# Kernel tuning notes

Hardware: AMD Instinct MI355X
Metric: run time of the kernel (lower is better)

## Reference

```python
import jax, jax.numpy as jnp
import numpy as np
from functools import partial

B, T, H, W = 8, 256, 64, 64
D_MODEL, N_LAYERS, D_STATE = 256, 6, 16
D_INNER = 2 * D_MODEL
DT_RANK = 16  # ceil(256/16)
D_CONV = 4
CNN_Z = 32


def setup_inputs() -> dict:
    key = jax.random.key(0)
    ks = iter(jax.random.split(key, 64))
    r = lambda shape, s=0.02: jax.random.normal(next(ks), shape, dtype=jnp.float32) * s
    inp = {
        'x': jax.random.normal(next(ks), (B, T, 1, H, W), dtype=jnp.float32),
        # frozen CNN spatial encoder (1->16->32->32, stride-2 convs, global avg pool)
        'cnn_w1': r((16, 1, 3, 3)), 'cnn_b1': jnp.zeros((16,)),
        'cnn_w2': r((32, 16, 3, 3)), 'cnn_b2': jnp.zeros((32,)),
        'cnn_w3': r((32, 32, 3, 3)), 'cnn_b3': jnp.zeros((32,)),
        # fc_s2t: 32 -> 256
        'fc_w': r((D_MODEL, CNN_Z)), 'fc_b': jnp.zeros((D_MODEL,)),
        # Mamba, stacked over layers
        'norm_w': jnp.ones((N_LAYERS, D_MODEL)),
        'in_proj_w': r((N_LAYERS, 2 * D_INNER, D_MODEL)),
        'conv1d_w': r((N_LAYERS, D_INNER, D_CONV)),
        'conv1d_b': jnp.zeros((N_LAYERS, D_INNER)),
        'x_proj_w': r((N_LAYERS, DT_RANK + 2 * D_STATE, D_INNER)),
        'dt_proj_w': r((N_LAYERS, D_INNER, DT_RANK)),
        'dt_proj_b': jnp.full((N_LAYERS, D_INNER), -4.6),  # softplus ~ 0.01
        'A_log': jnp.tile(jnp.log(jnp.arange(1, D_STATE + 1, dtype=jnp.float32))[None, None, :], (N_LAYERS, D_INNER, 1)),
        'Dp': jnp.ones((N_LAYERS, D_INNER)),
        'out_proj_w': r((N_LAYERS, D_MODEL, D_INNER)),
        'norm_f_w': jnp.ones((D_MODEL,)),
        # prediction head: 256 -> 64 -> 1
        'head_w1': r((D_MODEL // 4, D_MODEL)), 'head_b1': jnp.zeros((D_MODEL // 4,)),
        'head_w2': r((1, D_MODEL // 4)), 'head_b2': jnp.zeros((1,)),
    }
    return inp


def _conv2d(x, w, b, stride):
    y = jax.lax.conv_general_dilated(x, w, (stride, stride), 'SAME',
                                     dimension_numbers=('NCHW', 'OIHW', 'NCHW'))
    return jax.nn.relu(y + b[None, :, None, None])


def _rmsnorm(x, w, eps=1e-5):
    return x * jax.lax.rsqrt(jnp.mean(x * x, axis=-1, keepdims=True) + eps) * w


def _selective_scan(u, delta, A, Bm, Cm, Dvec):
    # u,delta: (B,L,E); A: (E,N); Bm,Cm: (B,L,N); D: (E,)
    deltaA = jnp.exp(delta[..., None] * A)                       # (B,L,E,N)
    deltaBu = delta[..., None] * Bm[:, :, None, :] * u[..., None]  # (B,L,E,N)

    def step(h, inputs):
        dA, dBu, c = inputs
        h = dA * h + dBu                    # (B,E,N)
        y = jnp.einsum('ben,bn->be', h, c)  # (B,E)
        return h, y

    h0 = jnp.zeros((u.shape[0], u.shape[2], A.shape[1]), u.dtype)
    xs = (deltaA.transpose(1, 0, 2, 3), deltaBu.transpose(1, 0, 2, 3), Cm.transpose(1, 0, 2))
    _, ys = jax.lax.scan(step, h0, xs)
    return ys.transpose(1, 0, 2) + u * Dvec  # (B,L,E)


def _mamba_block(x, nw, ipw, cw, cb, xpw, dpw, dpb, a_log, dvec, opw):
    b, l, d = x.shape
    xz = _rmsnorm(x, nw) @ ipw.T                 # (B,L,2E)
    xin, z = jnp.split(xz, 2, axis=-1)
    # causal depthwise conv1d, kernel 4
    xc = xin.transpose(0, 2, 1)                  # (B,E,L)
    xc = jax.lax.conv_general_dilated(xc, cw[:, None, :], (1,), [(D_CONV - 1, 0)],
                                      feature_group_count=D_INNER,
                                      dimension_numbers=('NCH', 'OIH', 'NCH'))
    xin = jax.nn.silu((xc + cb[None, :, None]).transpose(0, 2, 1))  # (B,L,E)
    dbc = xin @ xpw.T                             # (B,L,dtr+2N)
    dt, Bm, Cm = jnp.split(dbc, [DT_RANK, DT_RANK + D_STATE], axis=-1)
    delta = jax.nn.softplus(dt @ dpw.T + dpb)     # (B,L,E)
    A = -jnp.exp(a_log)                           # (E,N)
    y = _selective_scan(xin, delta, A, Bm, Cm, dvec)
    y = y * jax.nn.silu(z)
    return x + y @ opw.T


def reference(x, cnn_w1, cnn_b1, cnn_w2, cnn_b2, cnn_w3, cnn_b3, fc_w, fc_b,
              norm_w, in_proj_w, conv1d_w, conv1d_b, x_proj_w, dt_proj_w, dt_proj_b,
              A_log, Dp, out_proj_w, norm_f_w, head_w1, head_b1, head_w2, head_b2):
    b, t = x.shape[:2]
    # spatial encoder per frame
    f = x.reshape(b * t, 1, H, W)
    f = _conv2d(f, cnn_w1, cnn_b1, 2)
    f = _conv2d(f, cnn_w2, cnn_b2, 2)
    f = _conv2d(f, cnn_w3, cnn_b3, 2)
    z1 = jnp.mean(f, axis=(2, 3)).reshape(b, t, CNN_Z)   # (B,T,32)
    h = z1 @ fc_w.T + fc_b                                # (B,T,256)
    for i in range(N_LAYERS):
        h = _mamba_block(h, norm_w[i], in_proj_w[i], conv1d_w[i], conv1d_b[i],
                         x_proj_w[i], dt_proj_w[i], dt_proj_b[i], A_log[i], Dp[i], out_proj_w[i])
    z2 = _rmsnorm(h, norm_f_w)
    hh = jax.nn.gelu(z2 @ head_w1.T + head_b1)
    logits = hh @ head_w2.T + head_b2                     # (B,T,1)
    w = jax.nn.softmax(logits, axis=-2)
    w = w.at[:, 0, 0].set(0.0)
    return w
```

## Files before the change

kernel.cpp:

```cpp
#include <hip/hip_runtime.h>
#include <hip/hip_bf16.h>
#include <math.h>

#define Bb 8
#define Tt 256
#define DM 256
#define DI 512
#define NL 6
#define DS 16
#define DTR 16

#define OFF_H     0u
#define OFF_XZ    524288u
#define OFF_U     2621440u
#define OFF_DBC   3670016u
#define OFF_DELTA 3768320u
#define OFF_HH    4816896u
#define OFF_LOGIT 4947968u
#define OFF_XNB   4950016u
#define OFF_UB    5212160u
#define OFF_YBF   5736448u
#define OFF_WIP   6260736u
#define OFF_WXP   7047168u
#define OFF_WOP   7120896u

__device__ __forceinline__ float siluf(float x) { return x / (1.f + __expf(-x)); }

typedef __attribute__((ext_vector_type(8))) short bf16x8;
typedef __attribute__((ext_vector_type(4))) short bf16x4;
typedef __attribute__((ext_vector_type(4))) float f32x4;
typedef __attribute__((ext_vector_type(4))) unsigned int u32x4;

__device__ __forceinline__ unsigned short f2bf(float x) {
  unsigned u = __float_as_uint(x);
  u += 0x7FFFu + ((u >> 16) & 1u);
  return (unsigned short)(u >> 16);
}
__device__ __forceinline__ float bf2f(unsigned short u) {
  return __uint_as_float((unsigned)u << 16);
}
__device__ __forceinline__ float ldf(const float* p) { return *p; }
__device__ __forceinline__ float ldf(const unsigned short* p) { return bf2f(*p); }

__global__ __launch_bounds__(256) void cvt_bf16_kernel(const float* __restrict__ src,
                                                       unsigned short* __restrict__ dst,
                                                       int nvec) {
  int i = blockIdx.x * 256 + threadIdx.x;
  if (i < nvec) {
    float4 v = ((const float4*)src)[i];
    bf16x4 o;
    o[0] = (short)f2bf(v.x); o[1] = (short)f2bf(v.y);
    o[2] = (short)f2bf(v.z); o[3] = (short)f2bf(v.w);
    ((bf16x4*)dst)[i] = o;
  }
}

__global__ __launch_bounds__(256) void cnn_fc_mfma(
    const float* __restrict__ x,
    const float* __restrict__ w1, const float* __restrict__ b1,
    const float* __restrict__ w2, const float* __restrict__ b2,
    const float* __restrict__ w3, const float* __restrict__ b3,
    const float* __restrict__ fcw, const float* __restrict__ fcb,
    float* __restrict__ hout) {
  __shared__ __align__(16) unsigned short ldsu[31024];
  __shared__ float s_pool[32];
  const int tid = threadIdx.x;
  const int f = blockIdx.x;
  const int lane = tid & 63;
  const int lc = lane & 15;
  const int fq = lane >> 4;
  const int wv = tid >> 6;

  const int FR = 0;
  const int W2 = 0;
  const int C1 = 6400;
  const int C2 = 22800;
  const int W3 = 0;

  {
    const float* xin = x + (size_t)f * 4096;
#pragma unroll
    for (int r = 0; r < 4; ++r) {
      float4 v = ((const float4*)xin)[r * 256 + tid];
      bf16x4 o;
      o[0] = (short)f2bf(v.x); o[1] = (short)f2bf(v.y);
      o[2] = (short)f2bf(v.z); o[3] = (short)f2bf(v.w);
      *(bf16x4*)&ldsu[FR + (r * 256 + tid) * 4] = o;
    }
    if (tid < 8)  ((unsigned*)&ldsu[C1 + 1024 * 16])[tid] = 0u;
    if (tid < 16) ((unsigned*)&ldsu[C2 + 256 * 32])[tid] = 0u;
    if (tid < 32) s_pool[tid] = 0.f;
  }
  __syncthreads();

#pragma unroll
  for (int r = 0; r < 4; ++r) {
    int p = r * 256 + tid;
    int oy = p >> 5, ox = p & 31;
    float in9[9];
#pragma unroll
    for (int ky = 0; ky < 3; ++ky) {
      int iy = 2 * oy + ky;
#pragma unroll
      for (int kx = 0; kx < 3; ++kx) {
        int ix = 2 * ox + kx;
        in9[ky * 3 + kx] = (iy < 64 && ix < 64) ? bf2f(ldsu[FR + iy * 64 + ix]) : 0.f;
      }
    }
    bf16x8 o0, o1;
#pragma unroll
    for (int oc = 0; oc < 8; ++oc) {
      float s = b1[oc];
#pragma unroll
      for (int k = 0; k < 9; ++k) s += w1[oc * 9 + k] * in9[k];
      o0[oc] = (short)f2bf(fmaxf(s, 0.f));
    }
#pragma unroll
    for (int oc = 0; oc < 8; ++oc) {
      float s = b1[8 + oc];
#pragma unroll
      for (int k = 0; k < 9; ++k) s += w1[(8 + oc) * 9 + k] * in9[k];
      o1[oc] = (short)f2bf(fmaxf(s, 0.f));
    }
    *(bf16x8*)&ldsu[C1 + p * 16] = o0;
    *(bf16x8*)&ldsu[C1 + p * 16 + 8] = o1;
  }
  __syncthreads();

  for (int r = 0; r < 20; ++r) {
    int i = r * 256 + tid;
    int kt = i >> 10, rem = i & 1023;
    int oc = rem >> 5, k = rem & 31;
    int tap = 2 * kt + (k >> 4), ic = k & 15;
    float v = (tap < 9) ? w2[oc * 144 + ic * 9 + tap] : 0.f;
    ldsu[W2 + (kt * 32 + oc) * 40 + k] = f2bf(v);
  }
  __syncthreads();

  {
    f32x4 acc[2][4] = {};
    for (int kt = 0; kt < 5; ++kt) {
      bf16x8 a0 = *(const bf16x8*)&ldsu[W2 + (kt * 32 + lc) * 40 + fq * 8];
      bf16x8 a1 = *(const bf16x8*)&ldsu[W2 + (kt * 32 + 16 + lc) * 40 + fq * 8];
      int tap = 2 * kt + (fq >> 1);
      int t9 = (tap < 9) ? tap : 0;
      int ky = (t9 * 11) >> 5;
      int kx = t9 - ky * 3;
      int ix = 2 * lc + kx;
#pragma unroll
      for (int ni = 0; ni < 4; ++ni) {
        int nt = wv * 4 + ni;
        int iy = 2 * nt + ky;
        int ipos = (tap < 9 && iy < 32 && ix < 32) ? iy * 32 + ix : 1024;
        bf16x8 b = *(const bf16x8*)&ldsu[C1 + ipos * 16 + (fq & 1) * 8];
        acc[0][ni] = __builtin_amdgcn_mfma_f32_16x16x32_bf16(a0, b, acc[0][ni], 0, 0, 0);
        acc[1][ni] = __builtin_amdgcn_mfma_f32_16x16x32_bf16(a1, b, acc[1][ni], 0, 0, 0);
      }
    }
#pragma unroll
    for (int mi = 0; mi < 2; ++mi) {
      int oc0 = mi * 16 + fq * 4;
#pragma unroll
      for (int ni = 0; ni < 4; ++ni) {
        int pos = (wv * 4 + ni) * 16 + lc;
        bf16x4 o;
#pragma unroll
        for (int j = 0; j < 4; ++j)
          o[j] = (short)f2bf(fmaxf(acc[mi][ni][j] + b2[oc0 + j], 0.f));
        int g = mi * 4 + fq;
        int gp = ((((g >> 1) ^ ((pos >> 1) & 3)) << 1) | (g & 1));
        *(bf16x4*)&ldsu[C2 + pos * 32 + gp * 4] = o;
      }
    }
  }
  __syncthreads();

  for (int r = 0; r < 36; ++r) {
    int i = r * 256 + tid;
    int tap = i >> 10, rem = i & 1023;
    int oc = rem >> 5, ic = rem & 31;
    ldsu[W3 + (tap * 32 + oc) * 40 + ic] = f2bf(w3[oc * 288 + ic * 9 + tap]);
  }
  __syncthreads();

  {
    const int mh = wv >> 1, nb = wv & 1;
    f32x4 acc[2] = {};
#pragma unroll
    for (int tap = 0; tap < 9; ++tap) {
      const int ky = tap / 3, kx = tap % 3;
      bf16x8 a = *(const bf16x8*)&ldsu[W3 + (tap * 32 + mh * 16 + lc) * 40 + fq * 8];
#pragma unroll
      for (int ni = 0; ni < 2; ++ni) {
        int pos = (nb * 2 + ni) * 16 + lc;
        int py = pos >> 3, px = pos & 7;
        int iy = 2 * py + ky, ix = 2 * px + kx;
        int ipos = (iy < 16 && ix < 16) ? iy * 16 + ix : 256;
        int sp = fq ^ ((ipos >> 1) & 3);
        bf16x8 b = *(const bf16x8*)&ldsu[C2 + ipos * 32 + sp * 8];
        acc[ni] = __builtin_amdgcn_mfma_f32_16x16x32_bf16(a, b, acc[ni], 0, 0, 0);
      }
    }
    int oc0 = mh * 16 + fq * 4;
#pragma unroll
    for (int j = 0; j < 4; ++j) {
      float v = fmaxf(acc[0][j] + b3[oc0 + j], 0.f) +
                fmaxf(acc[1][j] + b3[oc0 + j], 0.f);
      v += __shfl_xor(v, 1);
      v += __shfl_xor(v, 2);
      v += __shfl_xor(v, 4);
      v += __shfl_xor(v, 8);
      if (lc == 0) atomicAdd(&s_pool[oc0 + j], v);
    }
  }
  __syncthreads();

  {
    float dot = 0.f;
#pragma unroll
    for (int k = 0; k < 32; ++k) dot += fcw[tid * 32 + k] * s_pool[k];
    hout[(size_t)f * 256 + tid] = fcb[tid] + dot * (1.f / 64.f);
  }
}

__global__ __launch_bounds__(256) void rmsnorm_kernel(const float* __restrict__ x,
                                                      const float* __restrict__ w,
                                                      unsigned short* __restrict__ ob) {
  __shared__ float red[4];
  int t = blockIdx.x, j = threadIdx.x;
  float v = x[(size_t)t * 256 + j];
  float s = v * v;
#pragma unroll
  for (int m = 32; m; m >>= 1) s += __shfl_xor(s, m);
  if ((j & 63) == 0) red[j >> 6] = s;
  __syncthreads();
  float tot = red[0] + red[1] + red[2] + red[3];
  float r = rsqrtf(tot * (1.f / 256.f) + 1e-5f);
  ob[(size_t)t * 256 + j] = f2bf(v * r * w[j]);
}

template <int ACT>
__global__ __launch_bounds__(256) void gemm_bb(const unsigned short* __restrict__ A,
                                               const unsigned short* __restrict__ W,
                                               float* __restrict__ C,
                                               int M, int N, int K) {
  __shared__ __align__(16) unsigned short sA[64 * 72];
  __shared__ __align__(16) unsigned short sW[64 * 72];
  const int tid = threadIdx.x;
  const int m0 = blockIdx.x * 64, n0 = blockIdx.y * 64;
  const int srow = tid >> 2, sseg = tid & 3;
  int wrow = n0 + srow; if (wrow >= N) wrow = 0;
  const unsigned short* gA = A + (size_t)(m0 + srow) * K + sseg * 16;
  const unsigned short* gW = W + (size_t)wrow * K + sseg * 16;
  const int wv = tid >> 6, wm = wv >> 1, wn = wv & 1;
  const int fr = tid & 15;
  const int fq = (tid >> 4) & 3;
  f32x4 acc[2][2] = {};

  const int NT = K >> 6;
  u32x4 ra0, ra1, rw0, rw1;
  ra0 = ((const u32x4*)gA)[0]; ra1 = ((const u32x4*)gA)[1];
  rw0 = ((const u32x4*)gW)[0]; rw1 = ((const u32x4*)gW)[1];
  *(u32x4*)&sA[srow * 72 + sseg * 16] = ra0;
  *(u32x4*)&sA[srow * 72 + sseg * 16 + 8] = ra1;
  *(u32x4*)&sW[srow * 72 + sseg * 16] = rw0;
  *(u32x4*)&sW[srow * 72 + sseg * 16 + 8] = rw1;
  __syncthreads();

  for (int kt = 0; kt < NT; ++kt) {
    if (kt + 1 < NT) {
      ra0 = ((const u32x4*)(gA + (kt + 1) * 64))[0];
      ra1 = ((const u32x4*)(gA + (kt + 1) * 64))[1];
      rw0 = ((const u32x4*)(gW + (kt + 1) * 64))[0];
      rw1 = ((const u32x4*)(gW + (kt + 1) * 64))[1];
    }
#pragma unroll
    for (int ks = 0; ks < 2; ++ks) {
      bf16x8 a0 = *(const bf16x8*)&sA[(wm * 32 + fr) * 72 + ks * 32 + fq * 8];
      bf16x8 a1 = *(const bf16x8*)&sA[(wm * 32 + 16 + fr) * 72 + ks * 32 + fq * 8];
      bf16x8 b0 = *(const bf16x8*)&sW[(wn * 32 + fr) * 72 + ks * 32 + fq * 8];
      bf16x8 b1 = *(const bf16x8*)&sW[(wn * 32 + 16 + fr) * 72 + ks * 32 + fq * 8];
      acc[0][0] = __builtin_amdgcn_mfma_f32_16x16x32_bf16(a0, b0, acc[0][0], 0, 0, 0);
      acc[0][1] = __builtin_amdgcn_mfma_f32_16x16x32_bf16(a0, b1, acc[0][1], 0, 0, 0);
      acc[1][0] = __builtin_amdgcn_mfma_f32_16x16x32_bf16(a1, b0, acc[1][0], 0, 0, 0);
      acc[1][1] = __builtin_amdgcn_mfma_f32_16x16x32_bf16(a1, b1, acc[1][1], 0, 0, 0);
    }
    __syncthreads();
    if (kt + 1 < NT) {
      *(u32x4*)&sA[srow * 72 + sseg * 16] = ra0;
      *(u32x4*)&sA[srow * 72 + sseg * 16 + 8] = ra1;
      *(u32x4*)&sW[srow * 72 + sseg * 16] = rw0;
      *(u32x4*)&sW[srow * 72 + sseg * 16 + 8] = rw1;
      __syncthreads();
    }
  }

#pragma unroll
  for (int mr = 0; mr < 2; ++mr) {
#pragma unroll
    for (int nr = 0; nr < 2; ++nr) {
      int n = n0 + wn * 32 + nr * 16 + fr;
      if (n < N) {
#pragma unroll
        for (int j = 0; j < 4; ++j) {
          int m = m0 + wm * 32 + mr * 16 + fq * 4 + j;
          size_t idx = (size_t)m * N + n;
          if (ACT == 2) C[idx] += acc[mr][nr][j];
          else C[idx] = acc[mr][nr][j];
        }
      }
    }
  }
}

template <int ACT, typename AT>
__global__ __launch_bounds__(256) void gemm_nt(const AT* __restrict__ A, int lda,
                                               const float* __restrict__ W,
                                               const float* __restrict__ bias,
                                               float* __restrict__ C,
                                               int M, int N, int K) {
  __shared__ __align__(16) float sA[16][68];
  __shared__ __align__(16) float sW[16][68];
  const int m0 = blockIdx.x * 64;
  const int n0 = blockIdx.y * 64;
  const int tid = threadIdx.x;
  const int lk = tid & 15, lm = tid >> 4;
  const int tx = tid & 15, ty = tid >> 4;
  float acc[4][4] = {};

  for (int k0 = 0; k0 < K; k0 += 16) {
#pragma unroll
    for (int p = 0; p < 4; ++p) {
      int m = p * 16 + lm;
      sA[lk][m] = ldf(&A[(size_t)(m0 + m) * lda + k0 + lk]);
    }
#pragma unroll
    for (int p = 0; p < 4; ++p) {
      int n = p * 16 + lm;
      sW[lk][n] = (n0 + n < N) ? W[(size_t)(n0 + n) * K + k0 + lk] : 0.f;
    }
    __syncthreads();
#pragma unroll
    for (int k = 0; k < 16; ++k) {
      float4 a = *(const float4*)&sA[k][ty * 4];
      float4 b = *(const float4*)&sW[k][tx * 4];
      acc[0][0] += a.x * b.x; acc[0][1] += a.x * b.y; acc[0][2] += a.x * b.z; acc[0][3] += a.x * b.w;
      acc[1][0] += a.y * b.x; acc[1][1] += a.y * b.y; acc[1][2] += a.y * b.z; acc[1][3] += a.y * b.w;
      acc[2][0] += a.z * b.x; acc[2][1] += a.z * b.y; acc[2][2] += a.z * b.z; acc[2][3] += a.z * b.w;
      acc[3][0] += a.w * b.x; acc[3][1] += a.w * b.y; acc[3][2] += a.w * b.z; acc[3][3] += a.w * b.w;
    }
    __syncthreads();
  }
#pragma unroll
  for (int i = 0; i < 4; ++i) {
    int m = m0 + ty * 4 + i;
#pragma unroll
    for (int j = 0; j < 4; ++j) {
      int n = n0 + tx * 4 + j;
      if (n < N) {
        float v = acc[i][j];
        if (ACT == 1) {
          v += bias[n];
          v = (v > 20.f) ? v : log1pf(__expf(v));
        } else if (ACT == 3) {
          v += bias[n];
          float t3 = v * v * v;
          v = 0.5f * v * (1.f + tanhf(0.7978845608028654f * (v + 0.044715f * t3)));
        }
        C[(size_t)m * N + n] = v;
      }
    }
  }
}

__global__ __launch_bounds__(256) void conv1d_silu_kernel(const float* __restrict__ xz,
                                                          const float* __restrict__ cw,
                                                          const float* __restrict__ cb,
                                                          float* __restrict__ u,
                                                          unsigned short* __restrict__ ub) {
  int idx = blockIdx.x * 256 + threadIdx.x;
  int e = idx & (DI - 1);
  int bt = idx >> 9;
  int t = bt & (Tt - 1);
  int b = bt >> 8;
  float s = cb[e];
#pragma unroll
  for (int j = 0; j < 4; ++j) {
    int tt = t - 3 + j;
    if (tt >= 0) s += cw[e * 4 + j] * xz[((size_t)(b * Tt + tt)) * (2 * DI) + e];
  }
  float v = siluf(s);
  u[idx] = v;
  ub[idx] = f2bf(v);
}

__global__ __launch_bounds__(1024) void scan_kernel(const float* __restrict__ delta,
                                                    const float* __restrict__ u,
                                                    const float* __restrict__ dbc,
                                                    const float* __restrict__ xz,
                                                    const float* __restrict__ A_log,
                                                    const float* __restrict__ Dp,
                                                    unsigned short* __restrict__ ybf) {
  __shared__ float sD[256][16];
  __shared__ float sU[256][16];
  __shared__ float sB[256][16];
  __shared__ float sC[256][16];
  __shared__ float sY[256][16];
  const int tid = threadIdx.x;
  const int b = blockIdx.x >> 5;
  const int e0 = (blockIdx.x & 31) << 4;
  const int chunk = tid >> 8;
  const int el = (tid >> 4) & 15;
  const int n = tid & 15;
  const int e = e0 + el;
  const float An = -__expf(A_log[e * 16 + n]);
  const float Dv = Dp[e];
  const size_t rowbase = (size_t)b * Tt;

#pragma unroll
  for (int k = 0; k < 4; ++k) {
    int idx = k * 1024 + tid;
    int row = idx >> 4, col = idx & 15;
    size_t g = (rowbase + row) * DI + e0 + col;
    size_t gb = (rowbase + row) * 48;
    sD[row][col] = delta[g];
    sU[row][col] = u[g];
    sB[row][col] = dbc[gb + 16 + col];
    sC[row][col] = dbc[gb + 32 + col];
  }
  __syncthreads();

  float h = 0.f, ap = 1.f;
  const int t0 = chunk * 64;
#pragma unroll 4
  for (int t = t0; t < t0 + 64; ++t) {
    float dv = sD[t][el];
    float dA = __expf(dv * An);
    h = dA * h + dv * sB[t][n] * sU[t][el];
    ap *= dA;
  }
  float* hloc   = &sY[0][0];
  float* aprod  = &sY[64][0];
  float* startH = &sY[128][0];
  const int sidx = el * 16 + n;
  hloc[chunk * 256 + sidx] = h;
  aprod[chunk * 256 + sidx] = ap;
  __syncthreads();

  if (chunk == 0) {
    float H = 0.f;
    startH[sidx] = 0.f;
#pragma unroll
    for (int c = 0; c < 3; ++c) {
      H = aprod[c * 256 + sidx] * H + hloc[c * 256 + sidx];
      startH[(c + 1) * 256 + sidx] = H;
    }
  }
  __syncthreads();
  float h2 = startH[chunk * 256 + sidx];
  __syncthreads();

#pragma unroll 4
  for (int t = t0; t < t0 + 64; ++t) {
    float dv = sD[t][el];
    float uv = sU[t][el];
    float dA = __expf(dv * An);
    h2 = dA * h2 + dv * sB[t][n] * uv;
    float p = h2 * sC[t][n];
    p += __shfl_xor(p, 1);
    p += __shfl_xor(p, 2);
    p += __shfl_xor(p, 4);
    p += __shfl_xor(p, 8);
    if (n == 0) sY[t][el] = p + uv * Dv;
  }
  __syncthreads();

#pragma unroll
  for (int k = 0; k < 4; ++k) {
    int idx = k * 1024 + tid;
    int t = idx >> 4, col = idx & 15;
    float zv = xz[(rowbase + t) * (2 * DI) + DI + e0 + col];
    ybf[(rowbase + t) * DI + e0 + col] = f2bf(sY[t][col] * siluf(zv));
  }
}

__global__ __launch_bounds__(256) void logits_kernel(const float* __restrict__ hh,
                                                     const float* __restrict__ w2,
                                                     const float* __restrict__ b2,
                                                     float* __restrict__ logit) {
  int t = blockIdx.x * 256 + threadIdx.x;
  float s = b2[0];
#pragma unroll
  for (int k = 0; k < 64; ++k) s += hh[(size_t)t * 64 + k] * w2[k];
  logit[t] = s;
}

__global__ __launch_bounds__(256) void softmax_kernel(const float* __restrict__ logit,
                                                      float* __restrict__ out) {
  __shared__ float redm[4], reds[4];
  int b = blockIdx.x, t = threadIdx.x;
  float v = logit[b * 256 + t];
  float m = v;
#pragma unroll
  for (int k = 32; k; k >>= 1) m = fmaxf(m, __shfl_xor(m, k));
  if ((t & 63) == 0) redm[t >> 6] = m;
  __syncthreads();
  m = fmaxf(fmaxf(redm[0], redm[1]), fmaxf(redm[2], redm[3]));
  float e = __expf(v - m);
  float s = e;
#pragma unroll
  for (int k = 32; k; k >>= 1) s += __shfl_xor(s, k);
  if ((t & 63) == 0) reds[t >> 6] = s;
  __syncthreads();
  s = reds[0] + reds[1] + reds[2] + reds[3];
  out[b * 256 + t] = (t == 0) ? 0.f : e / s;
}

extern "C" void kernel_launch(void* const* d_in, const int* in_sizes, int n_in,
                              void* d_out, int out_size, void* d_ws, size_t ws_size,
                              hipStream_t stream) {
  const float* x      = (const float*)d_in[0];
  const float* cnn_w1 = (const float*)d_in[1];
  const float* cnn_b1 = (const float*)d_in[2];
  const float* cnn_w2 = (const float*)d_in[3];
  const float* cnn_b2 = (const float*)d_in[4];
  const float* cnn_w3 = (const float*)d_in[5];
  const float* cnn_b3 = (const float*)d_in[6];
  const float* fc_w   = (const float*)d_in[7];
  const float* fc_b   = (const float*)d_in[8];
  const float* norm_w = (const float*)d_in[9];
  const float* ipw    = (const float*)d_in[10];
  const float* cw     = (const float*)d_in[11];
  const float* cb     = (const float*)d_in[12];
  const float* xpw    = (const float*)d_in[13];
  const float* dpw    = (const float*)d_in[14];
  const float* dpb    = (const float*)d_in[15];
  const float* A_log  = (const float*)d_in[16];
  const float* Dp     = (const float*)d_in[17];
  const float* opw    = (const float*)d_in[18];
  const float* nfw    = (const float*)d_in[19];
  const float* hw1    = (const float*)d_in[20];
  const float* hb1    = (const float*)d_in[21];
  const float* hw2    = (const float*)d_in[22];
  const float* hb2    = (const float*)d_in[23];

  float* ws    = (float*)d_ws;
  float* h     = ws + OFF_H;
  float* xz    = ws + OFF_XZ;
  float* u     = ws + OFF_U;
  float* dbc   = ws + OFF_DBC;
  float* delta = ws + OFF_DELTA;
  float* hh    = ws + OFF_HH;
  float* logit = ws + OFF_LOGIT;
  unsigned short* xnb = (unsigned short*)(ws + OFF_XNB);
  unsigned short* ub  = (unsigned short*)(ws + OFF_UB);
  unsigned short* ybf = (unsigned short*)(ws + OFF_YBF);
  unsigned short* wip = (unsigned short*)(ws + OFF_WIP);
  unsigned short* wxp = (unsigned short*)(ws + OFF_WXP);
  unsigned short* wop = (unsigned short*)(ws + OFF_WOP);

  cvt_bf16_kernel<<<1536, 256, 0, stream>>>(ipw, wip, NL * 2 * DI * DM / 4);
  cvt_bf16_kernel<<<144, 256, 0, stream>>>(xpw, wxp, NL * 48 * DI / 4);
  cvt_bf16_kernel<<<768, 256, 0, stream>>>(opw, wop, NL * DM * DI / 4);

  cnn_fc_mfma<<<Bb * Tt, 256, 0, stream>>>(x, cnn_w1, cnn_b1, cnn_w2, cnn_b2,
                                           cnn_w3, cnn_b3, fc_w, fc_b, h);

  for (int l = 0; l < NL; ++l) {
    rmsnorm_kernel<<<Bb * Tt, 256, 0, stream>>>(h, norm_w + l * DM, xnb);
    {
      dim3 g(32, 16);
      gemm_bb<0><<<g, 256, 0, stream>>>(xnb, wip + (size_t)l * 2 * DI * DM, xz,
                                        Bb * Tt, 2 * DI, DM);
    }
    conv1d_silu_kernel<<<(Bb * Tt * DI) / 256, 256, 0, stream>>>(
        xz, cw + l * DI * 4, cb + l * DI, u, ub);
    {
      dim3 g(32, 1);
      gemm_bb<0><<<g, 256, 0, stream>>>(ub, wxp + (size_t)l * 48 * DI, dbc,
                                        Bb * Tt, 48, DI);
    }
    {
      dim3 g(32, 8);
      gemm_nt<1, float><<<g, 256, 0, stream>>>(dbc, 48, dpw + (size_t)l * DI * DTR,
                                               dpb + l * DI, delta, Bb * Tt, DI, DTR);
    }
    scan_kernel<<<Bb * 32, 1024, 0, stream>>>(
        delta, u, dbc, xz, A_log + (size_t)l * DI * DS, Dp + l * DI, ybf);
    {
      dim3 g(32, 4);
      gemm_bb<2><<<g, 256, 0, stream>>>(ybf, wop + (size_t)l * DM * DI, h,
                                        Bb * Tt, DM, DI);
    }
  }

  rmsnorm_kernel<<<Bb * Tt, 256, 0, stream>>>(h, nfw, xnb);
  {
    dim3 g(32, 1);
    gemm_nt<3, unsigned short><<<g, 256, 0, stream>>>(xnb, DM, hw1, hb1, hh,
                                                      Bb * Tt, 64, DM);
  }
  logits_kernel<<<Bb * Tt / 256, 256, 0, stream>>>(hh, hw2, hb2, logit);
  softmax_kernel<<<Bb, 256, 0, stream>>>(logit, (float*)d_out);
}
```

Before: 639.6 us.

## Fuse rmsnorm into in_proj, dt_proj into scan, split-K x_proj and out_proj

Folds the per-layer RMSNorm into the in_proj GEMM prologue by computing the row scale in-kernel and applying it in the epilogue. x_proj becomes a 4-way split-K GEMM writing partial sums, which the scan kernel reduces before computing dt_proj plus softplus itself. This removes the separate delta and fp32 u buffers. out_proj becomes split-K with atomicAdd into the residual. The weight conversions are merged into one launch and logits plus softmax into one head kernel. The aim is fewer launches and less global traffic, at the cost of atomics (non-deterministic sums) and extra scan-kernel work.

```diff
diff --git a/kernel.cpp b/kernel.cpp
--- a/kernel.cpp
+++ b/kernel.cpp
@@ -12,17 +12,15 @@
 
 #define OFF_H     0u
 #define OFF_XZ    524288u
-#define OFF_U     2621440u
-#define OFF_DBC   3670016u
-#define OFF_DELTA 3768320u
-#define OFF_HH    4816896u
-#define OFF_LOGIT 4947968u
-#define OFF_XNB   4950016u
-#define OFF_UB    5212160u
-#define OFF_YBF   5736448u
-#define OFF_WIP   6260736u
-#define OFF_WXP   7047168u
-#define OFF_WOP   7120896u
+#define OFF_DBCP  2621440u
+#define OFF_HH    3014656u
+#define OFF_LOGIT 3145728u
+#define OFF_XNB   3147776u
+#define OFF_UB    3278848u
+#define OFF_YBF   3540992u
+#define OFF_WIP   3803136u
+#define OFF_WXP   4589568u
+#define OFF_WOP   4663296u
 
 __device__ __forceinline__ float siluf(float x) { return x / (1.f + __expf(-x)); }
 
@@ -42,17 +40,20 @@
 __device__ __forceinline__ float ldf(const float* p) { return *p; }
 __device__ __forceinline__ float ldf(const unsigned short* p) { return bf2f(*p); }
 
-__global__ __launch_bounds__(256) void cvt_bf16_kernel(const float* __restrict__ src,
-                                                       unsigned short* __restrict__ dst,
-                                                       int nvec) {
+__global__ __launch_bounds__(256) void cvt_all_kernel(
+    const float* __restrict__ s0, unsigned short* __restrict__ d0, int n0,
+    const float* __restrict__ s1, unsigned short* __restrict__ d1, int n1,
+    const float* __restrict__ s2, unsigned short* __restrict__ d2, int n2) {
   int i = blockIdx.x * 256 + threadIdx.x;
-  if (i < nvec) {
-    float4 v = ((const float4*)src)[i];
-    bf16x4 o;
-    o[0] = (short)f2bf(v.x); o[1] = (short)f2bf(v.y);
-    o[2] = (short)f2bf(v.z); o[3] = (short)f2bf(v.w);
-    ((bf16x4*)dst)[i] = o;
-  }
+  const float* s; unsigned short* d; int j = i;
+  if (j < n0) { s = s0; d = d0; }
+  else { j -= n0; if (j < n1) { s = s1; d = d1; }
+         else { j -= n1; if (j >= n2) return; s = s2; d = d2; } }
+  float4 v = ((const float4*)s)[j];
+  bf16x4 o;
+  o[0] = (short)f2bf(v.x); o[1] = (short)f2bf(v.y);
+  o[2] = (short)f2bf(v.z); o[3] = (short)f2bf(v.w);
+  ((bf16x4*)d)[j] = o;
 }
 
 __global__ __launch_bounds__(256) void cnn_fc_mfma(
@@ -239,25 +240,103 @@
   ob[(size_t)t * 256 + j] = f2bf(v * r * w[j]);
 }
 
-template <int ACT>
-__global__ __launch_bounds__(256) void gemm_bb(const unsigned short* __restrict__ A,
+__global__ __launch_bounds__(256) void gemm_rn(const float* __restrict__ H,
+                                               const float* __restrict__ nw,
                                                const unsigned short* __restrict__ W,
-                                               float* __restrict__ C,
-                                               int M, int N, int K) {
+                                               float* __restrict__ C) {
+  __shared__ __align__(16) unsigned short sA[64 * 260];
+  __shared__ __align__(16) unsigned short sW[64 * 72];
+  __shared__ float s_r[64];
+  const int tid = threadIdx.x;
+  const int m0 = blockIdx.x * 64, n0 = blockIdx.y * 64;
+  const int srow = tid >> 2, sseg = tid & 3;
+  {
+    const float4* gA4 = (const float4*)(H + (size_t)(m0 + srow) * 256 + sseg * 64);
+    const float4* nw4 = (const float4*)(nw + sseg * 64);
+    float ss = 0.f;
+#pragma unroll
+    for (int q = 0; q < 16; ++q) {
+      float4 v = gA4[q];
+      float4 wv = nw4[q];
+      ss += v.x * v.x + v.y * v.y + v.z * v.z + v.w * v.w;
+      bf16x4 o;
+      o[0] = (short)f2bf(v.x * wv.x); o[1] = (short)f2bf(v.y * wv.y);
+      o[2] = (short)f2bf(v.z * wv.z); o[3] = (short)f2bf(v.w * wv.w);
+      *(bf16x4*)&sA[srow * 260 + sseg * 64 + q * 4] = o;
+    }
+    ss += __shfl_xor(ss, 1);
+    ss += __shfl_xor(ss, 2);
+    if ((tid & 3) == 0) s_r[srow] = rsqrtf(ss * (1.f / 256.f) + 1e-5f);
+  }
+  const unsigned short* gW = W + (size_t)(n0 + srow) * 256 + sseg * 16;
+  u32x4 rw0 = ((const u32x4*)gW)[0];
+  u32x4 rw1 = ((const u32x4*)gW)[1];
+  *(u32x4*)&sW[srow * 72 + sseg * 16] = rw0;
+  *(u32x4*)&sW[srow * 72 + sseg * 16 + 8] = rw1;
+  __syncthreads();
+
+  const int wv = tid >> 6, wm = wv >> 1, wn = wv & 1;
+  const int fr = tid & 15;
+  const int fq = (tid >> 4) & 3;
+  f32x4 acc[2][2] = {};
+
+  for (int kt = 0; kt < 4; ++kt) {
+    if (kt < 3) {
+      rw0 = ((const u32x4*)(gW + (kt + 1) * 64))[0];
+      rw1 = ((const u32x4*)(gW + (kt + 1) * 64))[1];
+    }
+#pragma unroll
+    for (int ks = 0; ks < 2; ++ks) {
+      bf16x8 a0 = *(const bf16x8*)&sA[(wm * 32 + fr) * 260 + kt * 64 + ks * 32 + fq * 8];
+      bf16x8 a1 = *(const bf16x8*)&sA[(wm * 32 + 16 + fr) * 260 + kt * 64 + ks * 32 + fq * 8];
+      bf16x8 b0 = *(const bf16x8*)&sW[(wn * 32 + fr) * 72 + ks * 32 + fq * 8];
+      bf16x8 b1 = *(const bf16x8*)&sW[(wn * 32 + 16 + fr) * 72 + ks * 32 + fq * 8];
+      acc[0][0] = __builtin_amdgcn_mfma_f32_16x16x32_bf16(a0, b0, acc[0][0], 0, 0, 0);
+      acc[0][1] = __builtin_amdgcn_mfma_f32_16x16x32_bf16(a0, b1, acc[0][1], 0, 0, 0);
+      acc[1][0] = __builtin_amdgcn_mfma_f32_16x16x32_bf16(a1, b0, acc[1][0], 0, 0, 0);
+      acc[1][1] = __builtin_amdgcn_mfma_f32_16x16x32_bf16(a1, b1, acc[1][1], 0, 0, 0);
+    }
+    if (kt < 3) {
+      __syncthreads();
+      *(u32x4*)&sW[srow * 72 + sseg * 16] = rw0;
+      *(u32x4*)&sW[srow * 72 + sseg * 16 + 8] = rw1;
+      __syncthreads();
+    }
+  }
+
+#pragma unroll
+  for (int mr = 0; mr < 2; ++mr) {
+#pragma unroll
+    for (int nr = 0; nr < 2; ++nr) {
+      int n = n0 + wn * 32 + nr * 16 + fr;
+#pragma unroll
+      for (int j = 0; j < 4; ++j) {
+        int ml = wm * 32 + mr * 16 + fq * 4 + j;
+        C[(size_t)(m0 + ml) * 1024 + n] = acc[mr][nr][j] * s_r[ml];
+      }
+    }
+  }
+}
+
+__global__ __launch_bounds__(256) void gemm_bb_acc(const unsigned short* __restrict__ A,
+                                                   const unsigned short* __restrict__ W,
+                                                   float* __restrict__ C,
+                                                   int M, int N, int K) {
   __shared__ __align__(16) unsigned short sA[64 * 72];
   __shared__ __align__(16) unsigned short sW[64 * 72];
   const int tid = threadIdx.x;
   const int m0 = blockIdx.x * 64, n0 = blockIdx.y * 64;
+  const int ksz = K / (int)gridDim.z;
+  const int koff = blockIdx.z * ksz;
   const int srow = tid >> 2, sseg = tid & 3;
-  int wrow = n0 + srow; if (wrow >= N) wrow = 0;
-  const unsigned short* gA = A + (size_t)(m0 + srow) * K + sseg * 16;
-  const unsigned short* gW = W + (size_t)wrow * K + sseg * 16;
+  const unsigned short* gA = A + (size_t)(m0 + srow) * K + koff + sseg * 16;
+  const unsigned short* gW = W + (size_t)(n0 + srow) * K + koff + sseg * 16;
   const int wv = tid >> 6, wm = wv >> 1, wn = wv & 1;
   const int fr = tid & 15;
   const int fq = (tid >> 4) & 3;
   f32x4 acc[2][2] = {};
 
-  const int NT = K >> 6;
+  const int NT = ksz >> 6;
   u32x4 ra0, ra1, rw0, rw1;
   ra0 = ((const u32x4*)gA)[0]; ra1 = ((const u32x4*)gA)[1];
   rw0 = ((const u32x4*)gW)[0]; rw1 = ((const u32x4*)gW)[1];
@@ -300,16 +379,213 @@
 #pragma unroll
     for (int nr = 0; nr < 2; ++nr) {
       int n = n0 + wn * 32 + nr * 16 + fr;
-      if (n < N) {
+#pragma unroll
+      for (int j = 0; j < 4; ++j) {
+        int m = m0 + wm * 32 + mr * 16 + fq * 4 + j;
+        atomicAdd(&C[(size_t)m * N + n], acc[mr][nr][j]);
+      }
+    }
+  }
+}
+
+__global__ __launch_bounds__(256) void gemm_xp(const unsigned short* __restrict__ A,
+                                               const unsigned short* __restrict__ W,
+                                               float* __restrict__ Cp) {
+  __shared__ __align__(16) unsigned short sA[64 * 72];
+  __shared__ __align__(16) unsigned short sW[64 * 72];
+  const int tid = threadIdx.x;
+  const int m0 = blockIdx.x * 64;
+  const int koff = blockIdx.y * 128;
+  const int srow = tid >> 2, sseg = tid & 3;
+  int wrow = (srow < 48) ? srow : 0;
+  const unsigned short* gA = A + (size_t)(m0 + srow) * 512 + koff + sseg * 16;
+  const unsigned short* gW = W + (size_t)wrow * 512 + koff + sseg * 16;
+  const int wv = tid >> 6, wm = wv >> 1, wn = wv & 1;
+  const int fr = tid & 15;
+  const int fq = (tid >> 4) & 3;
+  f32x4 acc[2][2] = {};
+
+  u32x4 ra0, ra1, rw0, rw1;
+  ra0 = ((const u32x4*)gA)[0]; ra1 = ((const u32x4*)gA)[1];
+  rw0 = ((const u32x4*)gW)[0]; rw1 = ((const u32x4*)gW)[1];
+  *(u32x4*)&sA[srow * 72 + sseg * 16] = ra0;
+  *(u32x4*)&sA[srow * 72 + sseg * 16 + 8] = ra1;
+  *(u32x4*)&sW[srow * 72 + sseg * 16] = rw0;
+  *(u32x4*)&sW[srow * 72 + sseg * 16 + 8] = rw1;
+  __syncthreads();
+
+  for (int kt = 0; kt < 2; ++kt) {
+    if (kt == 0) {
+      ra0 = ((const u32x4*)(gA + 64))[0];
+      ra1 = ((const u32x4*)(gA + 64))[1];
+      rw0 = ((const u32x4*)(gW + 64))[0];
+      rw1 = ((const u32x4*)(gW + 64))[1];
+    }
+#pragma unroll
+    for (int ks = 0; ks < 2; ++ks) {
+      bf16x8 a0 = *(const bf16x8*)&sA[(wm * 32 + fr) * 72 + ks * 32 + fq * 8];
+      bf16x8 a1 = *(const bf16x8*)&sA[(wm * 32 + 16 + fr) * 72 + ks * 32 + fq * 8];
+      bf16x8 b0 = *(const bf16x8*)&sW[(wn * 32 + fr) * 72 + ks * 32 + fq * 8];
+      bf16x8 b1 = *(const bf16x8*)&sW[(wn * 32 + 16 + fr) * 72 + ks * 32 + fq * 8];
+      acc[0][0] = __builtin_amdgcn_mfma_f32_16x16x32_bf16(a0, b0, acc[0][0], 0, 0, 0);
+      acc[0][1] = __builtin_amdgcn_mfma_f32_16x16x32_bf16(a0, b1, acc[0][1], 0, 0, 0);
+      acc[1][0] = __builtin_amdgcn_mfma_f32_16x16x32_bf16(a1, b0, acc[1][0], 0, 0, 0);
+      acc[1][1] = __builtin_amdgcn_mfma_f32_16x16x32_bf16(a1, b1, acc[1][1], 0, 0, 0);
+    }
+    if (kt == 0) {
+      __syncthreads();
+      *(u32x4*)&sA[srow * 72 + sseg * 16] = ra0;
+      *(u32x4*)&sA[srow * 72 + sseg * 16 + 8] = ra1;
+      *(u32x4*)&sW[srow * 72 + sseg * 16] = rw0;
+      *(u32x4*)&sW[srow * 72 + sseg * 16 + 8] = rw1;
+      __syncthreads();
+    }
+  }
+
+  float* Co = Cp + (size_t)blockIdx.y * 2048 * 48;
+#pragma unroll
+  for (int mr = 0; mr < 2; ++mr) {
+#pragma unroll
+    for (int nr = 0; nr < 2; ++nr) {
+      int n = wn * 32 + nr * 16 + fr;
+      if (n < 48) {
 #pragma unroll
         for (int j = 0; j < 4; ++j) {
           int m = m0 + wm * 32 + mr * 16 + fq * 4 + j;
-          size_t idx = (size_t)m * N + n;
-          if (ACT == 2) C[idx] += acc[mr][nr][j];
-          else C[idx] = acc[mr][nr][j];
+          Co[(size_t)m * 48 + n] = acc[mr][nr][j];
         }
       }
     }
+  }
+}
+
+__global__ __launch_bounds__(256) void conv1d_silu_kernel(const float* __restrict__ xz,
+                                                          const float* __restrict__ cw,
+                                                          const float* __restrict__ cb,
+                                                          unsigned short* __restrict__ ub) {
+  int idx = blockIdx.x * 256 + threadIdx.x;
+  int e = idx & (DI - 1);
+  int bt = idx >> 9;
+  int t = bt & (Tt - 1);
+  int b = bt >> 8;
+  float s = cb[e];
+#pragma unroll
+  for (int j = 0; j < 4; ++j) {
+    int tt = t - 3 + j;
+    if (tt >= 0) s += cw[e * 4 + j] * xz[((size_t)(b * Tt + tt)) * (2 * DI) + e];
+  }
+  ub[idx] = f2bf(siluf(s));
+}
+
+__global__ __launch_bounds__(1024) void scan_kernel(const float* __restrict__ dbcp,
+                                                    const unsigned short* __restrict__ ub,
+                                                    const float* __restrict__ xz,
+                                                    const float* __restrict__ A_log,
+                                                    const float* __restrict__ Dp,
+                                                    const float* __restrict__ dpw,
+                                                    const float* __restrict__ dpb,
+                                                    unsigned short* __restrict__ ybf) {
+  __shared__ float sD[256][16];
+  __shared__ float sU[256][16];
+  __shared__ float sB[256][16];
+  __shared__ float sC[256][16];
+  __shared__ float sY[256][16];
+  __shared__ float s_dpwT[16][17];
+  __shared__ float s_dpb[16];
+  const int tid = threadIdx.x;
+  const int b = blockIdx.x >> 5;
+  const int e0 = (blockIdx.x & 31) << 4;
+  const int chunk = tid >> 8;
+  const int el = (tid >> 4) & 15;
+  const int n = tid & 15;
+  const int e = e0 + el;
+  const float An = -__expf(A_log[e * 16 + n]);
+  const float Dv = Dp[e];
+  const size_t rowbase = (size_t)b * Tt;
+
+  if (tid < 256) s_dpwT[tid & 15][tid >> 4] = dpw[(size_t)(e0 + (tid >> 4)) * DTR + (tid & 15)];
+  if (tid >= 256 && tid < 272) s_dpb[tid - 256] = dpb[e0 + tid - 256];
+
+#pragma unroll
+  for (int k = 0; k < 4; ++k) {
+    int idx = k * 1024 + tid;
+    int row = idx >> 4, col = idx & 15;
+    size_t gb = (rowbase + row) * 48;
+    float dt = 0.f, Bv = 0.f, Cv = 0.f;
+#pragma unroll
+    for (int kz = 0; kz < 4; ++kz) {
+      const float* p = dbcp + (size_t)kz * 2048 * 48 + gb;
+      dt += p[col]; Bv += p[16 + col]; Cv += p[32 + col];
+    }
+    sY[row][col] = dt;
+    sB[row][col] = Bv;
+    sC[row][col] = Cv;
+    sU[row][col] = bf2f(ub[(rowbase + row) * DI + e0 + col]);
+  }
+  __syncthreads();
+
+#pragma unroll
+  for (int k = 0; k < 4; ++k) {
+    int idx = k * 1024 + tid;
+    int t = idx >> 4, l = idx & 15;
+    float a = s_dpb[l];
+#pragma unroll
+    for (int kk = 0; kk < 16; ++kk) a += sY[t][kk] * s_dpwT[kk][l];
+    sD[t][l] = (a > 20.f) ? a : log1pf(__expf(a));
+  }
+  __syncthreads();
+
+  float h = 0.f, ap = 1.f;
+  const int t0 = chunk * 64;
+#pragma unroll 4
+  for (int t = t0; t < t0 + 64; ++t) {
+    float dv = sD[t][el];
+    float dA = __expf(dv * An);
+    h = dA * h + dv * sB[t][n] * sU[t][el];
+    ap *= dA;
+  }
+  float* hloc   = &sY[0][0];
+  float* aprod  = &sY[64][0];
+  float* startH = &sY[128][0];
+  const int sidx = el * 16 + n;
+  hloc[chunk * 256 + sidx] = h;
+  aprod[chunk * 256 + sidx] = ap;
+  __syncthreads();
+
+  if (chunk == 0) {
+    float H = 0.f;
+    startH[sidx] = 0.f;
+#pragma unroll
+    for (int c = 0; c < 3; ++c) {
+      H = aprod[c * 256 + sidx] * H + hloc[c * 256 + sidx];
+      startH[(c + 1) * 256 + sidx] = H;
+    }
+  }
+  __syncthreads();
+  float h2 = startH[chunk * 256 + sidx];
+  __syncthreads();
+
+#pragma unroll 4
+  for (int t = t0; t < t0 + 64; ++t) {
+    float dv = sD[t][el];
+    float uv = sU[t][el];
+    float dA = __expf(dv * An);
+    h2 = dA * h2 + dv * sB[t][n] * uv;
+    float p = h2 * sC[t][n];
+    p += __shfl_xor(p, 1);
+    p += __shfl_xor(p, 2);
+    p += __shfl_xor(p, 4);
+    p += __shfl_xor(p, 8);
+    if (n == 0) sY[t][el] = p + uv * Dv;
+  }
+  __syncthreads();
+
+#pragma unroll
+  for (int k = 0; k < 4; ++k) {
+    int idx = k * 1024 + tid;
+    int t = idx >> 4, col = idx & 15;
+    float zv = xz[(rowbase + t) * (2 * DI) + DI + e0 + col];
+    ybf[(rowbase + t) * DI + e0 + col] = f2bf(sY[t][col] * siluf(zv));
   }
 }
 
@@ -359,10 +635,7 @@
       int n = n0 + tx * 4 + j;
       if (n < N) {
         float v = acc[i][j];
-        if (ACT == 1) {
-          v += bias[n];
-          v = (v > 20.f) ? v : log1pf(__expf(v));
-        } else if (ACT == 3) {
+        if (ACT == 3) {
           v += bias[n];
           float t3 = v * v * v;
           v = 0.5f * v * (1.f + tanhf(0.7978845608028654f * (v + 0.044715f * t3)));
@@ -373,133 +646,20 @@
   }
 }
 
-__global__ __launch_bounds__(256) void conv1d_silu_kernel(const float* __restrict__ xz,
-                                                          const float* __restrict__ cw,
-                                                          const float* __restrict__ cb,
-                                                          float* __restrict__ u,
-                                                          unsigned short* __restrict__ ub) {
-  int idx = blockIdx.x * 256 + threadIdx.x;
-  int e = idx & (DI - 1);
-  int bt = idx >> 9;
-  int t = bt & (Tt - 1);
-  int b = bt >> 8;
-  float s = cb[e];
-#pragma unroll
-  for (int j = 0; j < 4; ++j) {
-    int tt = t - 3 + j;
-    if (tt >= 0) s += cw[e * 4 + j] * xz[((size_t)(b * Tt + tt)) * (2 * DI) + e];
-  }
-  float v = siluf(s);
-  u[idx] = v;
-  ub[idx] = f2bf(v);
-}
-
-__global__ __launch_bounds__(1024) void scan_kernel(const float* __restrict__ delta,
-                                                    const float* __restrict__ u,
-                                                    const float* __restrict__ dbc,
-                                                    const float* __restrict__ xz,
-                                                    const float* __restrict__ A_log,
-                                                    const float* __restrict__ Dp,
-                                                    unsigned short* __restrict__ ybf) {
-  __shared__ float sD[256][16];
-  __shared__ float sU[256][16];
-  __shared__ float sB[256][16];
-  __shared__ float sC[256][16];
-  __shared__ float sY[256][16];
-  const int tid = threadIdx.x;
-  const int b = blockIdx.x >> 5;
-  const int e0 = (blockIdx.x & 31) << 4;
-  const int chunk = tid >> 8;
-  const int el = (tid >> 4) & 15;
-  const int n = tid & 15;
-  const int e = e0 + el;
-  const float An = -__expf(A_log[e * 16 + n]);
-  const float Dv = Dp[e];
-  const size_t rowbase = (size_t)b * Tt;
-
-#pragma unroll
-  for (int k = 0; k < 4; ++k) {
-    int idx = k * 1024 + tid;
-    int row = idx >> 4, col = idx & 15;
-    size_t g = (rowbase + row) * DI + e0 + col;
-    size_t gb = (rowbase + row) * 48;
-    sD[row][col] = delta[g];
-    sU[row][col] = u[g];
-    sB[row][col] = dbc[gb + 16 + col];
-    sC[row][col] = dbc[gb + 32 + col];
-  }
-  __syncthreads();
-
-  float h = 0.f, ap = 1.f;
-  const int t0 = chunk * 64;
-#pragma unroll 4
-  for (int t = t0; t < t0 + 64; ++t) {
-    float dv = sD[t][el];
-    float dA = __expf(dv * An);
-    h = dA * h + dv * sB[t][n] * sU[t][el];
-    ap *= dA;
-  }
-  float* hloc   = &sY[0][0];
-  float* aprod  = &sY[64][0];
-  float* startH = &sY[128][0];
-  const int sidx = el * 16 + n;
-  hloc[chunk * 256 + sidx] = h;
-  aprod[chunk * 256 + sidx] = ap;
-  __syncthreads();
-
-  if (chunk == 0) {
-    float H = 0.f;
-    startH[sidx] = 0.f;
-#pragma unroll
-    for (int c = 0; c < 3; ++c) {
-      H = aprod[c * 256 + sidx] * H + hloc[c * 256 + sidx];
-      startH[(c + 1) * 256 + sidx] = H;
-    }
-  }
-  __syncthreads();
-  float h2 = startH[chunk * 256 + sidx];
-  __syncthreads();
-
-#pragma unroll 4
-  for (int t = t0; t < t0 + 64; ++t) {
-    float dv = sD[t][el];
-    float uv = sU[t][el];
-    float dA = __expf(dv * An);
-    h2 = dA * h2 + dv * sB[t][n] * uv;
-    float p = h2 * sC[t][n];
-    p += __shfl_xor(p, 1);
-    p += __shfl_xor(p, 2);
-    p += __shfl_xor(p, 4);
-    p += __shfl_xor(p, 8);
-    if (n == 0) sY[t][el] = p + uv * Dv;
-  }
-  __syncthreads();
-
-#pragma unroll
-  for (int k = 0; k < 4; ++k) {
-    int idx = k * 1024 + tid;
-    int t = idx >> 4, col = idx & 15;
-    float zv = xz[(rowbase + t) * (2 * DI) + DI + e0 + col];
-    ybf[(rowbase + t) * DI + e0 + col] = f2bf(sY[t][col] * siluf(zv));
-  }
-}
-
-__global__ __launch_bounds__(256) void logits_kernel(const float* __restrict__ hh,
-                                                     const float* __restrict__ w2,
-                                                     const float* __restrict__ b2,
-                                                     float* __restrict__ logit) {
-  int t = blockIdx.x * 256 + threadIdx.x;
-  float s = b2[0];
-#pragma unroll
-  for (int k = 0; k < 64; ++k) s += hh[(size_t)t * 64 + k] * w2[k];
-  logit[t] = s;
-}
-
-__global__ __launch_bounds__(256) void softmax_kernel(const float* __restrict__ logit,
-                                                      float* __restrict__ out) {
+__global__ __launch_bounds__(256) void head_kernel(const float* __restrict__ hh,
+                                                   const float* __restrict__ w2,
+                                                   const float* __restrict__ b2,
+                                                   float* __restrict__ out) {
   __shared__ float redm[4], reds[4];
   int b = blockIdx.x, t = threadIdx.x;
-  float v = logit[b * 256 + t];
+  const float4* row = (const float4*)(hh + ((size_t)b * 256 + t) * 64);
+  float v = b2[0];
+#pragma unroll
+  for (int q = 0; q < 16; ++q) {
+    float4 a = row[q];
+    float4 w = ((const float4*)w2)[q];
+    v += a.x * w.x + a.y * w.y + a.z * w.z + a.w * w.w;
+  }
   float m = v;
 #pragma unroll
   for (int k = 32; k; k >>= 1) m = fmaxf(m, __shfl_xor(m, k));
@@ -547,11 +707,9 @@
   float* ws    = (float*)d_ws;
   float* h     = ws + OFF_H;
   float* xz    = ws + OFF_XZ;
-  float* u     = ws + OFF_U;
-  float* dbc   = ws + OFF_DBC;
-  float* delta = ws + OFF_DELTA;
+  float* dbcp  = ws + OFF_DBCP;
   float* hh    = ws + OFF_HH;
-  float* logit = ws + OFF_LOGIT;
+  float* logit = ws + OFF_LOGIT;  (void)logit;
   unsigned short* xnb = (unsigned short*)(ws + OFF_XNB);
   unsigned short* ub  = (unsigned short*)(ws + OFF_UB);
   unsigned short* ybf = (unsigned short*)(ws + OFF_YBF);
@@ -559,38 +717,32 @@
   unsigned short* wxp = (unsigned short*)(ws + OFF_WXP);
   unsigned short* wop = (unsigned short*)(ws + OFF_WOP);
 
-  cvt_bf16_kernel<<<1536, 256, 0, stream>>>(ipw, wip, NL * 2 * DI * DM / 4);
-  cvt_bf16_kernel<<<144, 256, 0, stream>>>(xpw, wxp, NL * 48 * DI / 4);
-  cvt_bf16_kernel<<<768, 256, 0, stream>>>(opw, wop, NL * DM * DI / 4);
+  const int nv0 = NL * 2 * DI * DM / 4, nv1 = NL * 48 * DI / 4, nv2 = NL * DM * DI / 4;
+  cvt_all_kernel<<<(nv0 + nv1 + nv2 + 255) / 256, 256, 0, stream>>>(
+      ipw, wip, nv0, xpw, wxp, nv1, opw, wop, nv2);
 
   cnn_fc_mfma<<<Bb * Tt, 256, 0, stream>>>(x, cnn_w1, cnn_b1, cnn_w2, cnn_b2,
                                            cnn_w3, cnn_b3, fc_w, fc_b, h);
 
   for (int l = 0; l < NL; ++l) {
-    rmsnorm_kernel<<<Bb * Tt, 256, 0, stream>>>(h, norm_w + l * DM, xnb);
     {
       dim3 g(32, 16);
-      gemm_bb<0><<<g, 256, 0, stream>>>(xnb, wip + (size_t)l * 2 * DI * DM, xz,
-                                        Bb * Tt, 2 * DI, DM);
+      gemm_rn<<<g, 256, 0, stream>>>(h, norm_w + l * DM,
+                                     wip + (size_t)l * 2 * DI * DM, xz);
     }
     conv1d_silu_kernel<<<(Bb * Tt * DI) / 256, 256, 0, stream>>>(
-        xz, cw + l * DI * 4, cb + l * DI, u, ub);
-    {
-      dim3 g(32, 1);
-      gemm_bb<0><<<g, 256, 0, stream>>>(ub, wxp + (size_t)l * 48 * DI, dbc,
-                                        Bb * Tt, 48, DI);
-    }
-    {
-      dim3 g(32, 8);
-      gemm_nt<1, float><<<g, 256, 0, stream>>>(dbc, 48, dpw + (size_t)l * DI * DTR,
-                                               dpb + l * DI, delta, Bb * Tt, DI, DTR);
-    }
-    scan_kernel<<<Bb * 32, 1024, 0, stream>>>(
-        delta, u, dbc, xz, A_log + (size_t)l * DI * DS, Dp + l * DI, ybf);
+        xz, cw + l * DI * 4, cb + l * DI, ub);
     {
       dim3 g(32, 4);
-      gemm_bb<2><<<g, 256, 0, stream>>>(ybf, wop + (size_t)l * DM * DI, h,
-                                        Bb * Tt, DM, DI);
+      gemm_xp<<<g, 256, 0, stream>>>(ub, wxp + (size_t)l * 48 * DI, dbcp);
+    }
+    scan_kernel<<<Bb * 32, 1024, 0, stream>>>(
+        dbcp, ub, xz, A_log + (size_t)l * DI * DS, Dp + l * DI,
+        dpw + (size_t)l * DI * DTR, dpb + l * DI, ybf);
+    {
+      dim3 g(32, 4, 2);
+      gemm_bb_acc<<<g, 256, 0, stream>>>(ybf, wop + (size_t)l * DM * DI, h,
+                                         Bb * Tt, DM, DI);
     }
   }
 
@@ -600,6 +752,5 @@
     gemm_nt<3, unsigned short><<<g, 256, 0, stream>>>(xnb, DM, hw1, hb1, hh,
                                                       Bb * Tt, 64, DM);
   }
-  logits_kernel<<<Bb * Tt / 256, 256, 0, stream>>>(hh, hw2, hb2, logit);
-  softmax_kernel<<<Bb, 256, 0, stream>>>(logit, (float*)d_out);
-}
+  head_kernel<<<Bb, 256, 0, stream>>>(hh, hw2, hb2, (float*)d_out);
+}
```

After: 589.2 us. 7.9% less time.
